# Kernel optimization log

Hardware: AMD Instinct MI355X
Metric: run time of the kernel (lower is better)

Reference implementation:

```python
import jax, jax.numpy as jnp
import numpy as np

D_MODEL = 1024
NUM_HEADS = 16
KEY_DIM = 64
VALUE_DIM = 64
NEG_INF = jnp.float32(-1e30)


def setup_inputs() -> dict:
    key = jax.random.key(0)
    ks = jax.random.split(key, 10)
    B, S = 2, 2048
    lim = 1.0 / np.sqrt(D_MODEL)
    x = jax.random.normal(ks[0], (B, S, D_MODEL), dtype=jnp.float32)
    mask = jnp.ones((B, S), dtype=jnp.int32)  # pad mask: 1 = keep
    # stacked per-head linear params (Linear stores weight as [out, in])
    Wq = jax.random.uniform(ks[1], (NUM_HEADS, KEY_DIM, D_MODEL), jnp.float32, -lim, lim)
    bq = jax.random.uniform(ks[2], (NUM_HEADS, KEY_DIM), jnp.float32, -lim, lim)
    Wk = jax.random.uniform(ks[3], (NUM_HEADS, KEY_DIM, D_MODEL), jnp.float32, -lim, lim)
    bk = jax.random.uniform(ks[4], (NUM_HEADS, KEY_DIM), jnp.float32, -lim, lim)
    Wv = jax.random.uniform(ks[5], (NUM_HEADS, VALUE_DIM, D_MODEL), jnp.float32, -lim, lim)
    bv = jax.random.uniform(ks[6], (NUM_HEADS, VALUE_DIM), jnp.float32, -lim, lim)
    lim_o = 1.0 / np.sqrt(NUM_HEADS * VALUE_DIM)
    Wo = jax.random.uniform(ks[7], (D_MODEL, NUM_HEADS * VALUE_DIM), jnp.float32, -lim_o, lim_o)
    bo = jax.random.uniform(ks[8], (D_MODEL,), jnp.float32, -lim_o, lim_o)
    return {"x": x, "mask": mask, "Wq": Wq, "bq": bq, "Wk": Wk, "bk": bk,
            "Wv": Wv, "bv": bv, "Wo": Wo, "bo": bo}


def _mha(x, mask, Wq, bq, Wk, bk, Wv, bv, Wo, bo):
    B, S, _ = x.shape
    # per-head projections: [B, H, S, k]
    q = jnp.einsum('bsd,hkd->bhsk', x, Wq) + bq[None, :, None, :]
    k = jnp.einsum('bsd,hkd->bhsk', x, Wk) + bk[None, :, None, :]
    v = jnp.einsum('bsd,hvd->bhsv', x, Wv) + bv[None, :, None, :]
    scale = 1.0 / np.sqrt(KEY_DIM).astype(np.float32)
    scores = jnp.einsum('bhik,bhjk->bhij', q, k) * scale  # [B, H, S, S]
    # final mask = causal AND pad-row AND pad-col
    causal = jnp.tril(jnp.ones((S, S), dtype=bool))
    pad = mask.astype(bool)
    final = causal[None, None] & pad[:, None, :, None] & pad[:, None, None, :]
    masked = jnp.where(final, scores, NEG_INF)
    w = jax.nn.softmax(masked, axis=-1)
    w = jnp.where(final, w, 0.0)  # fully-masked rows -> zeros, matching loop impl
    out = jnp.einsum('bhij,bhjv->bhiv', w, v)            # [B, H, S, V]
    concat = out.transpose(0, 2, 1, 3).reshape(B, S, NUM_HEADS * VALUE_DIM)
    return concat @ Wo.T + bo


def reference(x, mask, Wq, bq, Wk, bk, Wv, bv, Wo, bo):
    return _mha(x, mask, Wq, bq, Wk, bk, Wv, bv, Wo, bo)
```

## Files before the change

kernel.cpp:

```cpp
#include <hip/hip_runtime.h>

#define SEQ 2048
#define NH 16
#define HD 64
#define DMODEL 1024

__device__ __forceinline__ unsigned int f2bf(float f) {
  unsigned int u = __float_as_uint(f);
  return ((u + 0x7fffu + ((u >> 16) & 1u)) >> 16) & 0xffffu;
}

__device__ __forceinline__ unsigned int pk2bf(float a, float b) {
  unsigned short ua = __builtin_bit_cast(unsigned short, (__bf16)a);
  unsigned short ub = __builtin_bit_cast(unsigned short, (__bf16)b);
  return (unsigned int)ua | ((unsigned int)ub << 16);
}

typedef __bf16 bf16x8 __attribute__((ext_vector_type(8)));
typedef float f32x4 __attribute__((ext_vector_type(4)));
typedef unsigned int uix4 __attribute__((ext_vector_type(4)));
typedef unsigned int uix2 __attribute__((ext_vector_type(2)));

__device__ __forceinline__ void gl2lds16(const unsigned short* g, unsigned short* l) {
  __builtin_amdgcn_global_load_lds(
      (const __attribute__((address_space(1))) unsigned int*)g,
      (__attribute__((address_space(3))) unsigned int*)l, 16, 0, 0);
}

__global__ __launch_bounds__(256) void cast_all_kernel(
    const float* __restrict__ x, const float* __restrict__ wq,
    const float* __restrict__ wk, const float* __restrict__ wv,
    const float* __restrict__ wo,
    unsigned short* __restrict__ xb, unsigned short* __restrict__ wqb,
    unsigned short* __restrict__ wkb, unsigned short* __restrict__ wvb,
    unsigned short* __restrict__ wob) {
  int idx = blockIdx.x * 256 + threadIdx.x;
  if (idx >= 1048576) return;
  const float* src;
  unsigned short* dst;
  int off;
  if (idx < 524288) {
    src = x; dst = xb; off = idx;
  } else {
    int t = idx - 524288;
    int w = t >> 17;
    off = t & 131071;
    src = (w == 0) ? wq : (w == 1) ? wk : (w == 2) ? wv : wo;
    dst = (w == 0) ? wqb : (w == 1) ? wkb : (w == 2) ? wvb : wob;
  }
  const float4* p = reinterpret_cast<const float4*>(src) + (size_t)off * 2;
  float4 a = p[0], b = p[1];
  uint4 o;
  o.x = f2bf(a.x) | (f2bf(a.y) << 16);
  o.y = f2bf(a.z) | (f2bf(a.w) << 16);
  o.z = f2bf(b.x) | (f2bf(b.y) << 16);
  o.w = f2bf(b.z) | (f2bf(b.w) << 16);
  reinterpret_cast<uint4*>(dst)[off] = o;
}

template <int MODE, int TM>
__global__ __launch_bounds__(256) void gemm128(
    const unsigned short* __restrict__ A, const unsigned short* __restrict__ B,
    const float* __restrict__ bias0, const float* __restrict__ bias1,
    const float* __restrict__ bias2, float* __restrict__ Cf,
    unsigned short* __restrict__ Qo, unsigned short* __restrict__ Ko,
    unsigned short* __restrict__ Vto, int Kdim) {
  constexpr int MT = TM / 32;
  __shared__ __align__(16) unsigned short As[TM * 64];
  __shared__ __align__(16) unsigned short Bs[128 * 64];
  const int tid = threadIdx.x;
  const int wave = tid >> 6, lane = tid & 63;
  const int wm = wave >> 1, wn = wave & 1;
  const int fr = lane & 15, quad = lane >> 4;
  const int fx = fr & 7;
  const int n0 = blockIdx.x * 128, m0 = blockIdx.y * TM;

  const int srowg = lane >> 3;
  const int schunk = (lane & 7) ^ (srowg & 7);
  const unsigned short* Abase =
      A + (size_t)(m0 + wave * (TM / 4) + srowg) * Kdim + schunk * 8;
  const unsigned short* Bbase =
      B + (size_t)(n0 + wave * 32 + srowg) * Kdim + schunk * 8;
  unsigned short* AsW = As + (wave * (TM / 4)) * 64;
  unsigned short* BsW = Bs + (wave * 32) * 64;

  f32x4 acc[MT][4];
#pragma unroll
  for (int mt = 0; mt < MT; ++mt)
#pragma unroll
    for (int nt = 0; nt < 4; ++nt) acc[mt][nt] = f32x4{0.f, 0.f, 0.f, 0.f};

  for (int k0 = 0; k0 < Kdim; k0 += 64) {
#pragma unroll
    for (int t = 0; t < TM / 32; ++t)
      gl2lds16(Abase + (size_t)(t * 8) * Kdim + k0, AsW + t * 8 * 64);
#pragma unroll
    for (int t = 0; t < 4; ++t)
      gl2lds16(Bbase + (size_t)(t * 8) * Kdim + k0, BsW + t * 8 * 64);
    __syncthreads();
#pragma unroll
    for (int ks = 0; ks < 2; ++ks) {
      bf16x8 af[MT], bfv[4];
#pragma unroll
      for (int mt = 0; mt < MT; ++mt)
        af[mt] = *reinterpret_cast<const bf16x8*>(
            As + (wm * (TM / 2) + mt * 16 + fr) * 64 + ((ks * 4 + quad) ^ fx) * 8);
#pragma unroll
      for (int nt = 0; nt < 4; ++nt)
        bfv[nt] = *reinterpret_cast<const bf16x8*>(
            Bs + (wn * 64 + nt * 16 + fr) * 64 + ((ks * 4 + quad) ^ fx) * 8);
#pragma unroll
      for (int mt = 0; mt < MT; ++mt)
#pragma unroll
        for (int nt = 0; nt < 4; ++nt)
          acc[mt][nt] = __builtin_amdgcn_mfma_f32_16x16x32_bf16(
              af[mt], bfv[nt], acc[mt][nt], 0, 0, 0);
    }
    __syncthreads();
  }

  if (MODE == 0) {
    const int seg = n0 >> 10;
    const float* bp = (seg == 0) ? bias0 : (seg == 1) ? bias1 : bias2;
    const float scale = (seg == 0) ? 0.1803368809f : 1.0f;
    unsigned short* QK = (seg == 0) ? Qo : Ko;
#pragma unroll
    for (int nt = 0; nt < 4; ++nt) {
      const int c = (n0 + wn * 64 + nt * 16 + fr) & 1023;
      const int h = c >> 6, d = c & 63;
      const float bs = bp[c];
#pragma unroll
      for (int mt = 0; mt < MT; ++mt) {
        const int mbase = m0 + wm * (TM / 2) + mt * 16 + quad * 4;
        const int b = mbase >> 11, s0 = mbase & 2047;
        if (seg < 2) {
          unsigned short* dst = QK + (((size_t)(b * NH + h)) * SEQ + s0) * HD + d;
#pragma unroll
          for (int r = 0; r < 4; ++r)
            dst[(size_t)r * HD] = (unsigned short)f2bf((acc[mt][nt][r] + bs) * scale);
        } else {
          uint2 pk;
          pk.x = pk2bf(acc[mt][nt][0] + bs, acc[mt][nt][1] + bs);
          pk.y = pk2bf(acc[mt][nt][2] + bs, acc[mt][nt][3] + bs);
          *reinterpret_cast<uint2*>(
              Vto + (((size_t)(b * NH + h)) * HD + d) * SEQ + s0) = pk;
        }
      }
    }
  } else {
#pragma unroll
    for (int nt = 0; nt < 4; ++nt) {
      const int cg = n0 + wn * 64 + nt * 16 + fr;
      const float bs = bias0[cg];
#pragma unroll
      for (int mt = 0; mt < MT; ++mt) {
        const int mbase = m0 + wm * (TM / 2) + mt * 16 + quad * 4;
#pragma unroll
        for (int r = 0; r < 4; ++r)
          Cf[(size_t)(mbase + r) * DMODEL + cg] = acc[mt][nt][r] + bs;
      }
    }
  }
}

__global__ __launch_bounds__(256, 4) void attn_mfma_kernel(
    const unsigned short* __restrict__ Qg, const unsigned short* __restrict__ Kg,
    const unsigned short* __restrict__ Vtg, const int* __restrict__ mask,
    unsigned short* __restrict__ concat) {
  const int w = blockIdx.x >> 8;
  const int c = blockIdx.x & 255;
  const int gg = c >> 5;
  const int bh = c & 31;
  const int ib = (w == 0) ? (31 - gg) : (w == 1) ? gg : (w == 2) ? (23 - gg) : (8 + gg);
  const int b = bh >> 4, h = bh & 15;
  const int tid = threadIdx.x;
  const int wave = tid >> 6, lane = tid & 63;
  const int quad = lane >> 4, fr = lane & 15;
  const int fx = fr & 7;

  __shared__ __align__(16) unsigned short Ks[2][64 * 64];
  __shared__ __align__(16) unsigned short Vts[2][64 * 64];

  const unsigned short* Qb = Qg + ((size_t)bh * SEQ) * HD;
  const unsigned short* Kb = Kg + ((size_t)bh * SEQ) * HD;
  const unsigned short* Vtb = Vtg + ((size_t)bh * HD) * SEQ;
  const int* maskb = mask + b * SEQ;

  bool badl = false;
  {
    const int4* mp4 = reinterpret_cast<const int4*>(maskb);
#pragma unroll
    for (int u = 0; u < 8; ++u) {
      int4 v = mp4[lane * 8 + u];
      badl |= !(v.x && v.y && v.z && v.w);
    }
  }
  const unsigned long long bm = __ballot(badl);

  const int ir = ib * 64 + wave * 16 + fr;
  const bf16x8 q0 = *reinterpret_cast<const bf16x8*>(Qb + (size_t)ir * HD + quad * 8);
  const bf16x8 q1 = *reinterpret_cast<const bf16x8*>(Qb + (size_t)ir * HD + quad * 8 + 32);
  const int padi = maskb[ir];

  f32x4 o[4];
#pragma unroll
  for (int vt = 0; vt < 4; ++vt) o[vt] = f32x4{0.f, 0.f, 0.f, 0.f};
  float mr = -1e20f;
  float lq = 0.f;

  const int srow8 = lane >> 3;
  const int sch8 = (lane & 7) ^ (srow8 & 7);
  const int kprow = (wave >> 1) * 32 + ((srow8 >> 2)) * 8 + (wave & 1) * 4 + (srow8 & 3);
  const unsigned short* Kcol = Kb + sch8 * 8;
  const unsigned short* Vsrc = Vtb + (size_t)(wave * 16 + srow8) * SEQ + sch8 * 8;
  const int cA0 = (quad ^ fx) * 8;
  const int cA1 = ((quad + 4) ^ fx) * 8;

  {
    unsigned short* KsW = Ks[0] + (wave * 16) * 64;
    unsigned short* VtsW = Vts[0] + (wave * 16) * 64;
#pragma unroll
    for (int t = 0; t < 2; ++t) {
      gl2lds16(Kcol + (size_t)(kprow + t * 16) * HD, KsW + t * 8 * 64);
      gl2lds16(Vsrc + (size_t)(t * 8) * SEQ, VtsW + t * 8 * 64);
    }
  }

  for (int jc = 0; jc <= ib; ++jc) {
    __syncthreads();
    if (jc < ib) {
      const int jn = (jc + 1) * 64;
      unsigned short* KsW = Ks[(jc + 1) & 1] + (wave * 16) * 64;
      unsigned short* VtsW = Vts[(jc + 1) & 1] + (wave * 16) * 64;
#pragma unroll
      for (int t = 0; t < 2; ++t) {
        gl2lds16(Kcol + (size_t)(jn + kprow + t * 16) * HD, KsW + t * 8 * 64);
        gl2lds16(Vsrc + (size_t)(t * 8) * SEQ + jn, VtsW + t * 8 * 64);
      }
    }
    const unsigned short* Kcur = Ks[jc & 1];
    const unsigned short* Vcur = Vts[jc & 1];
    const int j0 = jc * 64;
    const bool tb = ((bm >> (2 * jc)) & 3ull) != 0ull;

    f32x4 st[4];
    __builtin_amdgcn_s_setprio(1);
#pragma unroll
    for (int jt = 0; jt < 4; ++jt) {
      bf16x8 ka0 = *reinterpret_cast<const bf16x8*>(&Kcur[(jt * 16 + fr) * 64 + cA0]);
      bf16x8 ka1 = *reinterpret_cast<const bf16x8*>(&Kcur[(jt * 16 + fr) * 64 + cA1]);
      st[jt] = f32x4{0.f, 0.f, 0.f, 0.f};
      st[jt] = __builtin_amdgcn_mfma_f32_16x16x32_bf16(ka0, q0, st[jt], 0, 0, 0);
      st[jt] = __builtin_amdgcn_mfma_f32_16x16x32_bf16(ka1, q1, st[jt], 0, 0, 0);
    }
    __builtin_amdgcn_s_setprio(0);

    if (tb) {
      const int4* mp = reinterpret_cast<const int4*>(maskb + j0);
#pragma unroll
      for (int jt = 0; jt < 4; ++jt) {
        const int4 mv = mp[(jt >> 1) * 8 + quad * 2 + (jt & 1)];
        if (mv.x == 0) st[jt][0] = -1e30f;
        if (mv.y == 0) st[jt][1] = -1e30f;
        if (mv.z == 0) st[jt][2] = -1e30f;
        if (mv.w == 0) st[jt][3] = -1e30f;
      }
    }
    if (jc == ib) {
#pragma unroll
      for (int jt = 0; jt < 4; ++jt) {
        const int jb = j0 + (jt >> 1) * 32 + quad * 8 + (jt & 1) * 4;
#pragma unroll
        for (int r = 0; r < 4; ++r)
          if (jb + r > ir) st[jt][r] = -1e30f;
      }
    }

    float tmax = -1e30f;
#pragma unroll
    for (int jt = 0; jt < 4; ++jt)
#pragma unroll
      for (int r = 0; r < 4; ++r) tmax = fmaxf(tmax, st[jt][r]);
    tmax = fmaxf(tmax, __shfl_xor(tmax, 16));
    {
      uix2 rr = __builtin_amdgcn_permlane32_swap(__float_as_uint(tmax),
                                                 __float_as_uint(tmax), false, false);
      tmax = fmaxf(__uint_as_float(rr.x), __uint_as_float(rr.y));
    }
    if (jc == 0) mr = fmaxf(tmax, -1e20f);

    unsigned int pw[8];
#pragma unroll
    for (int jt = 0; jt < 4; ++jt) {
      float p0 = __builtin_amdgcn_exp2f(fminf(st[jt][0] - mr, 60.f));
      float p1 = __builtin_amdgcn_exp2f(fminf(st[jt][1] - mr, 60.f));
      float p2 = __builtin_amdgcn_exp2f(fminf(st[jt][2] - mr, 60.f));
      float p3 = __builtin_amdgcn_exp2f(fminf(st[jt][3] - mr, 60.f));
      lq += (p0 + p1) + (p2 + p3);
      pw[2 * jt] = pk2bf(p0, p1);
      pw[2 * jt + 1] = pk2bf(p2, p3);
    }
    const bf16x8 pa0 = __builtin_bit_cast(bf16x8, uix4{pw[0], pw[1], pw[2], pw[3]});
    const bf16x8 pa1 = __builtin_bit_cast(bf16x8, uix4{pw[4], pw[5], pw[6], pw[7]});

    __builtin_amdgcn_s_setprio(1);
#pragma unroll
    for (int vt = 0; vt < 4; ++vt) {
      bf16x8 vb0 = *reinterpret_cast<const bf16x8*>(&Vcur[(vt * 16 + fr) * 64 + cA0]);
      bf16x8 vb1 = *reinterpret_cast<const bf16x8*>(&Vcur[(vt * 16 + fr) * 64 + cA1]);
      o[vt] = __builtin_amdgcn_mfma_f32_16x16x32_bf16(vb0, pa0, o[vt], 0, 0, 0);
      o[vt] = __builtin_amdgcn_mfma_f32_16x16x32_bf16(vb1, pa1, o[vt], 0, 0, 0);
    }
    __builtin_amdgcn_s_setprio(0);

    if (jc > 0) {
      const bool upd = __ballot(tmax > mr + 8.f) != 0ull;
      if (upd) {
        const float mn = fmaxf(mr, tmax);
        const float corr = __builtin_amdgcn_exp2f(mr - mn);
        mr = mn;
        lq *= corr;
#pragma unroll
        for (int vt = 0; vt < 4; ++vt) {
          o[vt][0] *= corr; o[vt][1] *= corr; o[vt][2] *= corr; o[vt][3] *= corr;
        }
      }
    }
  }

  float lr = lq;
  lr += __shfl_xor(lr, 16);
  lr += __shfl_xor(lr, 32);
  const float inv = (padi != 0 && lr > 0.f) ? 1.f / lr : 0.f;
  unsigned short* orow = concat + ((size_t)(b * SEQ + ir)) * DMODEL + h * HD;
#pragma unroll
  for (int vt = 0; vt < 4; ++vt) {
    uint2 pk;
    pk.x = pk2bf(o[vt][0] * inv, o[vt][1] * inv);
    pk.y = pk2bf(o[vt][2] * inv, o[vt][3] * inv);
    *reinterpret_cast<uint2*>(orow + vt * 16 + quad * 4) = pk;
  }
}

extern "C" void kernel_launch(void* const* d_in, const int* in_sizes, int n_in,
                              void* d_out, int out_size, void* d_ws, size_t ws_size,
                              hipStream_t stream) {
  (void)in_sizes; (void)n_in; (void)out_size;
  const float* x  = (const float*)d_in[0];
  const int* mask = (const int*)d_in[1];
  const float* Wq = (const float*)d_in[2];
  const float* bq = (const float*)d_in[3];
  const float* Wk = (const float*)d_in[4];
  const float* bk = (const float*)d_in[5];
  const float* Wv = (const float*)d_in[6];
  const float* bv = (const float*)d_in[7];
  const float* Wo = (const float*)d_in[8];
  const float* bo = (const float*)d_in[9];
  float* out = (float*)d_out;

  char* ws = (char*)d_ws;
  if (ws_size < (48ull << 20)) return;
  unsigned short* xb  = (unsigned short*)(ws);
  unsigned short* wqb = (unsigned short*)(ws + (8ull  << 20));
  unsigned short* wkb = (unsigned short*)(ws + (10ull << 20));
  unsigned short* wvb = (unsigned short*)(ws + (12ull << 20));
  unsigned short* wob = (unsigned short*)(ws + (14ull << 20));
  unsigned short* Qb  = (unsigned short*)(ws + (16ull << 20));
  unsigned short* Kb  = (unsigned short*)(ws + (24ull << 20));
  unsigned short* Vtb = (unsigned short*)(ws + (32ull << 20));
  unsigned short* cb  = (unsigned short*)(ws + (40ull << 20));

  cast_all_kernel<<<4096, 256, 0, stream>>>(x, Wq, Wk, Wv, Wo, xb, wqb, wkb, wvb, wob);

  gemm128<0, 128><<<dim3(24, 32), 256, 0, stream>>>(xb, wqb, bq, bk, bv,
                                                    nullptr, Qb, Kb, Vtb, 1024);

  attn_mfma_kernel<<<1024, 256, 0, stream>>>(Qb, Kb, Vtb, mask, cb);

  gemm128<1, 64><<<dim3(8, 64), 256, 0, stream>>>(cb, wob, bo, nullptr, nullptr,
                                                  out, nullptr, nullptr, nullptr, 1024);
}
```

Baseline: 192.5 us.

## Double-buffer LDS tiles in GEMM to overlap global loads with MFMA

The projection GEMM now keeps two LDS buffers for the A and B tiles. It issues the async global-to-LDS loads for the next K step before computing on the current one, so memory traffic overlaps the MFMA work. The sync at the end of each iteration goes away, leaving one barrier per step. This doubles LDS use per block, which may lower occupancy.

```diff
diff --git a/kernel.cpp b/kernel.cpp
--- a/kernel.cpp
+++ b/kernel.cpp
@@ -66,8 +66,8 @@
     unsigned short* __restrict__ Qo, unsigned short* __restrict__ Ko,
     unsigned short* __restrict__ Vto, int Kdim) {
   constexpr int MT = TM / 32;
-  __shared__ __align__(16) unsigned short As[TM * 64];
-  __shared__ __align__(16) unsigned short Bs[128 * 64];
+  __shared__ __align__(16) unsigned short As[2][TM * 64];
+  __shared__ __align__(16) unsigned short Bs[2][128 * 64];
   const int tid = threadIdx.x;
   const int wave = tid >> 6, lane = tid & 63;
   const int wm = wave >> 1, wn = wave & 1;
@@ -81,8 +81,8 @@
       A + (size_t)(m0 + wave * (TM / 4) + srowg) * Kdim + schunk * 8;
   const unsigned short* Bbase =
       B + (size_t)(n0 + wave * 32 + srowg) * Kdim + schunk * 8;
-  unsigned short* AsW = As + (wave * (TM / 4)) * 64;
-  unsigned short* BsW = Bs + (wave * 32) * 64;
+  const int awoff = (wave * (TM / 4)) * 64;
+  const int bwoff = (wave * 32) * 64;
 
   f32x4 acc[MT][4];
 #pragma unroll
@@ -90,25 +90,40 @@
 #pragma unroll
     for (int nt = 0; nt < 4; ++nt) acc[mt][nt] = f32x4{0.f, 0.f, 0.f, 0.f};
 
-  for (int k0 = 0; k0 < Kdim; k0 += 64) {
-#pragma unroll
-    for (int t = 0; t < TM / 32; ++t)
-      gl2lds16(Abase + (size_t)(t * 8) * Kdim + k0, AsW + t * 8 * 64);
-#pragma unroll
-    for (int t = 0; t < 4; ++t)
-      gl2lds16(Bbase + (size_t)(t * 8) * Kdim + k0, BsW + t * 8 * 64);
+#pragma unroll
+  for (int t = 0; t < TM / 32; ++t)
+    gl2lds16(Abase + (size_t)(t * 8) * Kdim, As[0] + awoff + t * 8 * 64);
+#pragma unroll
+  for (int t = 0; t < 4; ++t)
+    gl2lds16(Bbase + (size_t)(t * 8) * Kdim, Bs[0] + bwoff + t * 8 * 64);
+
+  const int nk = Kdim >> 6;
+  for (int kk = 0; kk < nk; ++kk) {
     __syncthreads();
+    if (kk + 1 < nk) {
+      const int k0n = (kk + 1) * 64;
+      unsigned short* An = As[(kk + 1) & 1] + awoff;
+      unsigned short* Bn = Bs[(kk + 1) & 1] + bwoff;
+#pragma unroll
+      for (int t = 0; t < TM / 32; ++t)
+        gl2lds16(Abase + (size_t)(t * 8) * Kdim + k0n, An + t * 8 * 64);
+#pragma unroll
+      for (int t = 0; t < 4; ++t)
+        gl2lds16(Bbase + (size_t)(t * 8) * Kdim + k0n, Bn + t * 8 * 64);
+    }
+    const unsigned short* Acur = As[kk & 1];
+    const unsigned short* Bcur = Bs[kk & 1];
 #pragma unroll
     for (int ks = 0; ks < 2; ++ks) {
       bf16x8 af[MT], bfv[4];
 #pragma unroll
       for (int mt = 0; mt < MT; ++mt)
         af[mt] = *reinterpret_cast<const bf16x8*>(
-            As + (wm * (TM / 2) + mt * 16 + fr) * 64 + ((ks * 4 + quad) ^ fx) * 8);
+            Acur + (wm * (TM / 2) + mt * 16 + fr) * 64 + ((ks * 4 + quad) ^ fx) * 8);
 #pragma unroll
       for (int nt = 0; nt < 4; ++nt)
         bfv[nt] = *reinterpret_cast<const bf16x8*>(
-            Bs + (wn * 64 + nt * 16 + fr) * 64 + ((ks * 4 + quad) ^ fx) * 8);
+            Bcur + (wn * 64 + nt * 16 + fr) * 64 + ((ks * 4 + quad) ^ fx) * 8);
 #pragma unroll
       for (int mt = 0; mt < MT; ++mt)
 #pragma unroll
@@ -116,7 +131,6 @@
           acc[mt][nt] = __builtin_amdgcn_mfma_f32_16x16x32_bf16(
               af[mt], bfv[nt], acc[mt][nt], 0, 0, 0);
     }
-    __syncthreads();
   }
 
   if (MODE == 0) {
```

New measurement: 192.6 us. About the same (+0.1%).

## Fuse fp32-to-bf16 casting into the projection GEMM tile loads

Applied to the files above, without the earlier changes.

Removes the separate cast kernel. The QKV and output GEMMs now read fp32 inputs and weights directly, convert them to bf16 in registers and write them into LDS. This saves a full pass of writes and re-reads of bf16 copies plus one kernel launch. The cost is twice the global read bytes per tile, which is read repeatedly across the grid, and loads that go through registers instead of direct global-to-LDS loads, which may expose more latency.

```diff
diff --git a/kernel.cpp b/kernel.cpp
--- a/kernel.cpp
+++ b/kernel.cpp
@@ -27,138 +27,186 @@
       (__attribute__((address_space(3))) unsigned int*)l, 16, 0, 0);
 }
 
-__global__ __launch_bounds__(256) void cast_all_kernel(
-    const float* __restrict__ x, const float* __restrict__ wq,
-    const float* __restrict__ wk, const float* __restrict__ wv,
-    const float* __restrict__ wo,
-    unsigned short* __restrict__ xb, unsigned short* __restrict__ wqb,
-    unsigned short* __restrict__ wkb, unsigned short* __restrict__ wvb,
-    unsigned short* __restrict__ wob) {
-  int idx = blockIdx.x * 256 + threadIdx.x;
-  if (idx >= 1048576) return;
-  const float* src;
-  unsigned short* dst;
-  int off;
-  if (idx < 524288) {
-    src = x; dst = xb; off = idx;
-  } else {
-    int t = idx - 524288;
-    int w = t >> 17;
-    off = t & 131071;
-    src = (w == 0) ? wq : (w == 1) ? wk : (w == 2) ? wv : wo;
-    dst = (w == 0) ? wqb : (w == 1) ? wkb : (w == 2) ? wvb : wob;
-  }
-  const float4* p = reinterpret_cast<const float4*>(src) + (size_t)off * 2;
-  float4 a = p[0], b = p[1];
-  uint4 o;
-  o.x = f2bf(a.x) | (f2bf(a.y) << 16);
-  o.y = f2bf(a.z) | (f2bf(a.w) << 16);
-  o.z = f2bf(b.x) | (f2bf(b.y) << 16);
-  o.w = f2bf(b.z) | (f2bf(b.w) << 16);
-  reinterpret_cast<uint4*>(dst)[off] = o;
-}
-
-template <int MODE, int TM>
-__global__ __launch_bounds__(256) void gemm128(
-    const unsigned short* __restrict__ A, const unsigned short* __restrict__ B,
-    const float* __restrict__ bias0, const float* __restrict__ bias1,
-    const float* __restrict__ bias2, float* __restrict__ Cf,
+__device__ __forceinline__ void cvt_write8(float4 a, float4 b, unsigned short* lds) {
+  uix4 o;
+  o.x = pk2bf(a.x, a.y); o.y = pk2bf(a.z, a.w);
+  o.z = pk2bf(b.x, b.y); o.w = pk2bf(b.z, b.w);
+  *reinterpret_cast<uix4*>(lds) = o;
+}
+
+
+__global__ __launch_bounds__(256) void gemm_qkv(
+    const float* __restrict__ X, const float* __restrict__ Wq,
+    const float* __restrict__ Wk, const float* __restrict__ Wv,
+    const float* __restrict__ bq, const float* __restrict__ bk,
+    const float* __restrict__ bv,
     unsigned short* __restrict__ Qo, unsigned short* __restrict__ Ko,
-    unsigned short* __restrict__ Vto, int Kdim) {
-  constexpr int MT = TM / 32;
-  __shared__ __align__(16) unsigned short As[TM * 64];
+    unsigned short* __restrict__ Vto) {
+  __shared__ __align__(16) unsigned short As[128 * 64];
   __shared__ __align__(16) unsigned short Bs[128 * 64];
   const int tid = threadIdx.x;
   const int wave = tid >> 6, lane = tid & 63;
   const int wm = wave >> 1, wn = wave & 1;
   const int fr = lane & 15, quad = lane >> 4;
   const int fx = fr & 7;
-  const int n0 = blockIdx.x * 128, m0 = blockIdx.y * TM;
-
-  const int srowg = lane >> 3;
-  const int schunk = (lane & 7) ^ (srowg & 7);
-  const unsigned short* Abase =
-      A + (size_t)(m0 + wave * (TM / 4) + srowg) * Kdim + schunk * 8;
-  const unsigned short* Bbase =
-      B + (size_t)(n0 + wave * 32 + srowg) * Kdim + schunk * 8;
-  unsigned short* AsW = As + (wave * (TM / 4)) * 64;
-  unsigned short* BsW = Bs + (wave * 32) * 64;
-
-  f32x4 acc[MT][4];
-#pragma unroll
-  for (int mt = 0; mt < MT; ++mt)
+  const int n0 = blockIdx.x * 128, m0 = blockIdx.y * 128;
+  const int seg = n0 >> 10;
+  const float* W = (seg == 0) ? Wq : (seg == 1) ? Wk : Wv;
+  const float* bp = (seg == 0) ? bq : (seg == 1) ? bk : bv;
+
+  const int sr = lane >> 3;
+  const int sch = (lane & 7) ^ (sr & 7);
+  const float* Ag = X + (size_t)(m0 + wave * 32 + sr) * 1024 + sch * 8;
+  const float* Bg = W + (size_t)((n0 & 1023) + wave * 32 + sr) * 1024 + sch * 8;
+  unsigned short* AsW = As + (wave * 32 + sr) * 64 + (lane & 7) * 8;
+  unsigned short* BsW = Bs + (wave * 32 + sr) * 64 + (lane & 7) * 8;
+
+  f32x4 acc[4][4];
+#pragma unroll
+  for (int mt = 0; mt < 4; ++mt)
 #pragma unroll
     for (int nt = 0; nt < 4; ++nt) acc[mt][nt] = f32x4{0.f, 0.f, 0.f, 0.f};
 
-  for (int k0 = 0; k0 < Kdim; k0 += 64) {
-#pragma unroll
-    for (int t = 0; t < TM / 32; ++t)
-      gl2lds16(Abase + (size_t)(t * 8) * Kdim + k0, AsW + t * 8 * 64);
-#pragma unroll
-    for (int t = 0; t < 4; ++t)
-      gl2lds16(Bbase + (size_t)(t * 8) * Kdim + k0, BsW + t * 8 * 64);
+  for (int k0 = 0; k0 < 1024; k0 += 64) {
+    float4 ra[4][2];
+#pragma unroll
+    for (int t = 0; t < 4; ++t) {
+      const float* g = Ag + (size_t)(t * 8) * 1024 + k0;
+      ra[t][0] = *reinterpret_cast<const float4*>(g);
+      ra[t][1] = *reinterpret_cast<const float4*>(g + 4);
+    }
     __syncthreads();
 #pragma unroll
+    for (int t = 0; t < 4; ++t) cvt_write8(ra[t][0], ra[t][1], AsW + t * 8 * 64);
+    {
+      float4 rb[4][2];
+#pragma unroll
+      for (int t = 0; t < 4; ++t) {
+        const float* g = Bg + (size_t)(t * 8) * 1024 + k0;
+        rb[t][0] = *reinterpret_cast<const float4*>(g);
+        rb[t][1] = *reinterpret_cast<const float4*>(g + 4);
+      }
+#pragma unroll
+      for (int t = 0; t < 4; ++t) cvt_write8(rb[t][0], rb[t][1], BsW + t * 8 * 64);
+    }
+    __syncthreads();
+#pragma unroll
     for (int ks = 0; ks < 2; ++ks) {
-      bf16x8 af[MT], bfv[4];
-#pragma unroll
-      for (int mt = 0; mt < MT; ++mt)
+      bf16x8 af[4], bfv[4];
+#pragma unroll
+      for (int mt = 0; mt < 4; ++mt)
         af[mt] = *reinterpret_cast<const bf16x8*>(
-            As + (wm * (TM / 2) + mt * 16 + fr) * 64 + ((ks * 4 + quad) ^ fx) * 8);
+            As + (wm * 64 + mt * 16 + fr) * 64 + ((ks * 4 + quad) ^ fx) * 8);
 #pragma unroll
       for (int nt = 0; nt < 4; ++nt)
         bfv[nt] = *reinterpret_cast<const bf16x8*>(
             Bs + (wn * 64 + nt * 16 + fr) * 64 + ((ks * 4 + quad) ^ fx) * 8);
 #pragma unroll
-      for (int mt = 0; mt < MT; ++mt)
+      for (int mt = 0; mt < 4; ++mt)
 #pragma unroll
         for (int nt = 0; nt < 4; ++nt)
           acc[mt][nt] = __builtin_amdgcn_mfma_f32_16x16x32_bf16(
               af[mt], bfv[nt], acc[mt][nt], 0, 0, 0);
     }
+  }
+
+  const float scale = (seg == 0) ? 0.1803368809f : 1.0f;
+  unsigned short* QK = (seg == 0) ? Qo : Ko;
+#pragma unroll
+  for (int nt = 0; nt < 4; ++nt) {
+    const int c = (n0 + wn * 64 + nt * 16 + fr) & 1023;
+    const int h = c >> 6, d = c & 63;
+    const float bs = bp[c];
+#pragma unroll
+    for (int mt = 0; mt < 4; ++mt) {
+      const int mbase = m0 + wm * 64 + mt * 16 + quad * 4;
+      const int b = mbase >> 11, s0 = mbase & 2047;
+      if (seg < 2) {
+        unsigned short* dst = QK + (((size_t)(b * NH + h)) * SEQ + s0) * HD + d;
+#pragma unroll
+        for (int r = 0; r < 4; ++r)
+          dst[(size_t)r * HD] = (unsigned short)f2bf((acc[mt][nt][r] + bs) * scale);
+      } else {
+        uint2 pk;
+        pk.x = pk2bf(acc[mt][nt][0] + bs, acc[mt][nt][1] + bs);
+        pk.y = pk2bf(acc[mt][nt][2] + bs, acc[mt][nt][3] + bs);
+        *reinterpret_cast<uint2*>(
+            Vto + (((size_t)(b * NH + h)) * HD + d) * SEQ + s0) = pk;
+      }
+    }
+  }
+}
+
+__global__ __launch_bounds__(256) void gemm_out(
+    const unsigned short* __restrict__ A, const float* __restrict__ Wo,
+    const float* __restrict__ bo, float* __restrict__ Cf) {
+  __shared__ __align__(16) unsigned short As[64 * 64];
+  __shared__ __align__(16) unsigned short Bs[128 * 64];
+  const int tid = threadIdx.x;
+  const int wave = tid >> 6, lane = tid & 63;
+  const int wm = wave >> 1, wn = wave & 1;
+  const int fr = lane & 15, quad = lane >> 4;
+  const int fx = fr & 7;
+  const int n0 = blockIdx.x * 128, m0 = blockIdx.y * 64;
+
+  const int sr = lane >> 3;
+  const int sch = (lane & 7) ^ (sr & 7);
+  const unsigned short* Abase = A + (size_t)(m0 + wave * 16 + sr) * 1024 + sch * 8;
+  const float* Bg = Wo + (size_t)(n0 + wave * 32 + sr) * 1024 + sch * 8;
+  unsigned short* AsD = As + (wave * 16) * 64;
+  unsigned short* BsW = Bs + (wave * 32 + sr) * 64 + (lane & 7) * 8;
+
+  f32x4 acc[2][4];
+#pragma unroll
+  for (int mt = 0; mt < 2; ++mt)
+#pragma unroll
+    for (int nt = 0; nt < 4; ++nt) acc[mt][nt] = f32x4{0.f, 0.f, 0.f, 0.f};
+
+  for (int k0 = 0; k0 < 1024; k0 += 64) {
+    float4 rb[4][2];
+#pragma unroll
+    for (int t = 0; t < 4; ++t) {
+      const float* g = Bg + (size_t)(t * 8) * 1024 + k0;
+      rb[t][0] = *reinterpret_cast<const float4*>(g);
+      rb[t][1] = *reinterpret_cast<const float4*>(g + 4);
+    }
     __syncthreads();
-  }
-
-  if (MODE == 0) {
-    const int seg = n0 >> 10;
-    const float* bp = (seg == 0) ? bias0 : (seg == 1) ? bias1 : bias2;
-    const float scale = (seg == 0) ? 0.1803368809f : 1.0f;
-    unsigned short* QK = (seg == 0) ? Qo : Ko;
-#pragma unroll
-    for (int nt = 0; nt < 4; ++nt) {
-      const int c = (n0 + wn * 64 + nt * 16 + fr) & 1023;
-      const int h = c >> 6, d = c & 63;
-      const float bs = bp[c];
-#pragma unroll
-      for (int mt = 0; mt < MT; ++mt) {
-        const int mbase = m0 + wm * (TM / 2) + mt * 16 + quad * 4;
-        const int b = mbase >> 11, s0 = mbase & 2047;
-        if (seg < 2) {
-          unsigned short* dst = QK + (((size_t)(b * NH + h)) * SEQ + s0) * HD + d;
-#pragma unroll
-          for (int r = 0; r < 4; ++r)
-            dst[(size_t)r * HD] = (unsigned short)f2bf((acc[mt][nt][r] + bs) * scale);
-        } else {
-          uint2 pk;
-          pk.x = pk2bf(acc[mt][nt][0] + bs, acc[mt][nt][1] + bs);
-          pk.y = pk2bf(acc[mt][nt][2] + bs, acc[mt][nt][3] + bs);
-          *reinterpret_cast<uint2*>(
-              Vto + (((size_t)(b * NH + h)) * HD + d) * SEQ + s0) = pk;
-        }
-      }
-    }
-  } else {
-#pragma unroll
-    for (int nt = 0; nt < 4; ++nt) {
-      const int cg = n0 + wn * 64 + nt * 16 + fr;
-      const float bs = bias0[cg];
-#pragma unroll
-      for (int mt = 0; mt < MT; ++mt) {
-        const int mbase = m0 + wm * (TM / 2) + mt * 16 + quad * 4;
-#pragma unroll
-        for (int r = 0; r < 4; ++r)
-          Cf[(size_t)(mbase + r) * DMODEL + cg] = acc[mt][nt][r] + bs;
-      }
+#pragma unroll
+    for (int t = 0; t < 2; ++t)
+      gl2lds16(Abase + (size_t)(t * 8) * 1024 + k0, AsD + t * 8 * 64);
+#pragma unroll
+    for (int t = 0; t < 4; ++t) cvt_write8(rb[t][0], rb[t][1], BsW + t * 8 * 64);
+    __syncthreads();
+#pragma unroll
+    for (int ks = 0; ks < 2; ++ks) {
+      bf16x8 af[2], bfv[4];
+#pragma unroll
+      for (int mt = 0; mt < 2; ++mt)
+        af[mt] = *reinterpret_cast<const bf16x8*>(
+            As + (wm * 32 + mt * 16 + fr) * 64 + ((ks * 4 + quad) ^ fx) * 8);
+#pragma unroll
+      for (int nt = 0; nt < 4; ++nt)
+        bfv[nt] = *reinterpret_cast<const bf16x8*>(
+            Bs + (wn * 64 + nt * 16 + fr) * 64 + ((ks * 4 + quad) ^ fx) * 8);
+#pragma unroll
+      for (int mt = 0; mt < 2; ++mt)
+#pragma unroll
+        for (int nt = 0; nt < 4; ++nt)
+          acc[mt][nt] = __builtin_amdgcn_mfma_f32_16x16x32_bf16(
+              af[mt], bfv[nt], acc[mt][nt], 0, 0, 0);
+    }
+  }
+
+#pragma unroll
+  for (int nt = 0; nt < 4; ++nt) {
+    const int cg = n0 + wn * 64 + nt * 16 + fr;
+    const float bs = bo[cg];
+#pragma unroll
+    for (int mt = 0; mt < 2; ++mt) {
+      const int mbase = m0 + wm * 32 + mt * 16 + quad * 4;
+#pragma unroll
+      for (int r = 0; r < 4; ++r)
+        Cf[(size_t)(mbase + r) * DMODEL + cg] = acc[mt][nt][r] + bs;
     }
   }
 }
@@ -360,23 +408,15 @@
 
   char* ws = (char*)d_ws;
   if (ws_size < (48ull << 20)) return;
-  unsigned short* xb  = (unsigned short*)(ws);
-  unsigned short* wqb = (unsigned short*)(ws + (8ull  << 20));
-  unsigned short* wkb = (unsigned short*)(ws + (10ull << 20));
-  unsigned short* wvb = (unsigned short*)(ws + (12ull << 20));
-  unsigned short* wob = (unsigned short*)(ws + (14ull << 20));
   unsigned short* Qb  = (unsigned short*)(ws + (16ull << 20));
   unsigned short* Kb  = (unsigned short*)(ws + (24ull << 20));
   unsigned short* Vtb = (unsigned short*)(ws + (32ull << 20));
   unsigned short* cb  = (unsigned short*)(ws + (40ull << 20));
 
-  cast_all_kernel<<<4096, 256, 0, stream>>>(x, Wq, Wk, Wv, Wo, xb, wqb, wkb, wvb, wob);
-
-  gemm128<0, 128><<<dim3(24, 32), 256, 0, stream>>>(xb, wqb, bq, bk, bv,
-                                                    nullptr, Qb, Kb, Vtb, 1024);
+  gemm_qkv<<<dim3(24, 32), 256, 0, stream>>>(x, Wq, Wk, Wv, bq, bk, bv,
+                                             Qb, Kb, Vtb);
 
   attn_mfma_kernel<<<1024, 256, 0, stream>>>(Qb, Kb, Vtb, mask, cb);
 
-  gemm128<1, 64><<<dim3(8, 64), 256, 0, stream>>>(cb, wob, bo, nullptr, nullptr,
-                                                  out, nullptr, nullptr, nullptr, 1024);
-}
+  gemm_out<<<dim3(8, 64), 256, 0, stream>>>(cb, Wo, bo, out);
+}
```

New measurement: 214.6 us. +11.5%, slower.
